# Kernel optimization log

Measured on AMD Instinct MI355X. Metric: run time of the kernel, lower is better.

## Reference

```python
import jax, jax.numpy as jnp
import numpy as np

OLD_W, OLD_H = 224, 224   # raster image spatial size (originalShape[2:])
NEW_W, NEW_H = 28, 28     # feature-grid spatial size (newShape[2:])
B, N_SV, HID = 64, 63, 512  # batch, surrounding agents (N-1), LSTM encoder hidden
POS_SCALE = 250.0         # some positions exceed OLD_W to exercise validity masks


def setup_inputs() -> dict:
    key = jax.random.key(0)
    k1, k2, k3 = jax.random.split(key, 3)
    svPositionsAtT0 = jax.random.uniform(k1, (B, N_SV, 3), dtype=jnp.float32) * POS_SCALE
    svEncoding = jax.random.normal(k2, (B, N_SV, HID), dtype=jnp.float32)
    lengths = jax.random.randint(k3, (B,), 0, N_SV, dtype=jnp.int32)
    return {"svPositionsAtT0": svPositionsAtT0, "svEncoding": svEncoding, "lengths": lengths}


def reference(svPositionsAtT0, svEncoding, lengths):
    # Faithful vectorized form of rawToRasterScaleSocialState:
    # sequential per-agent max-writes into a zero-initialized grid == scatter-max.
    b_, n_, hid = svEncoding.shape
    x = svPositionsAtT0[..., 0]                     # (B, N)
    y = svPositionsAtT0[..., 1]
    xIdx = (x * NEW_W / OLD_W).astype(jnp.int32)    # trunc toward zero, as .long()
    yIdx = (y * NEW_H / OLD_H).astype(jnp.int32)
    agent_ids = jnp.arange(n_, dtype=lengths.dtype)[None, :]
    mask = (lengths[:, None] > agent_ids) & (xIdx < NEW_W) & (yIdx < NEW_H)  # (B, N)
    # Invalid agents: write 0 (no-op since grid init is 0 and writes are max-with-0)
    enc = jnp.where(mask[..., None], svEncoding, 0.0)          # (B, N, HID)
    xI = jnp.clip(xIdx, 0, NEW_W - 1)
    yI = jnp.clip(yIdx, 0, NEW_H - 1)
    bI = jnp.broadcast_to(jnp.arange(b_)[:, None], (b_, n_))
    grid = jnp.zeros((b_, hid, NEW_W, NEW_H), dtype=svEncoding.dtype)
    grid = grid.at[bI.ravel(), :, xI.ravel(), yI.ravel()].max(enc.reshape(b_ * n_, hid))
    return grid
```

## Files before the change

kernel.cpp:

```cpp
#include <hip/hip_runtime.h>
#include <hip/hip_bf16.h>

#define NSV    63
#define HID    512
#define GW     28
#define GH     28
#define CELLS  (GW * GH)
#define HCHUNK 16
#define NTHREADS 256
#define NF4    (HCHUNK * CELLS / 4)
#define F4ROW  (CELLS / 4)

__global__ __launch_bounds__(NTHREADS)
void scatter_grid_kernel(const float* __restrict__ pos,
                         const float* __restrict__ enc,
                         const int*   __restrict__ lengths,
                         float*       __restrict__ out) {
    const int b      = blockIdx.y;
    const int h_base = blockIdx.x * HCHUNK;
    const int t      = threadIdx.x;

    __shared__ unsigned long long mask_s[CELLS];
    __shared__ float enc_s[NSV * HCHUNK];

    for (int c = t; c < CELLS; c += NTHREADS) mask_s[c] = 0ull;

    {
        const int n = t >> 2;
        const int q = t & 3;
        if (n < NSV) {
            const float4 v = ((const float4*)(enc + ((size_t)b * NSV + n) * HID + h_base))[q];
            ((float4*)(enc_s + n * HCHUNK))[q] = v;
        }
    }
    __syncthreads();

    if (t < NSV) {
        const float x = pos[((size_t)b * NSV + t) * 3 + 0];
        const float y = pos[((size_t)b * NSV + t) * 3 + 1];
        const int len = lengths[b];
        const int xi = (int)(x * 28.0f / 224.0f);
        const int yi = (int)(y * 28.0f / 224.0f);
        if ((t < len) && (xi < GW) && (yi < GH)) {
            const int xc = min(max(xi, 0), GW - 1);
            const int yc = min(max(yi, 0), GH - 1);
            atomicOr(&mask_s[xc * GH + yc], 1ull << t);
        }
    }
    __syncthreads();

    float4* d4 = (float4*)(out + ((size_t)b * HID + h_base) * CELLS);
    for (int i = t; i < NF4; i += NTHREADS) {
        const int h = i / F4ROW;
        const int c = (i - h * F4ROW) * 4;
        float4 v = make_float4(0.f, 0.f, 0.f, 0.f);
        #pragma unroll
        for (int j = 0; j < 4; ++j) {
            unsigned long long m = mask_s[c + j];
            float val = 0.f;
            while (m) {
                const int n = __ffsll(m) - 1;
                m &= m - 1;
                val = fmaxf(val, enc_s[n * HCHUNK + h]);
            }
            (&v.x)[j] = val;
        }
        d4[i] = v;
    }
}

extern "C" void kernel_launch(void* const* d_in, const int* in_sizes, int n_in,
                              void* d_out, int out_size, void* d_ws, size_t ws_size,
                              hipStream_t stream) {
    const float* pos     = (const float*)d_in[0];
    const float* enc     = (const float*)d_in[1];
    const int*   lengths = (const int*)d_in[2];
    float*       out     = (float*)d_out;

    const int B = in_sizes[2];

    dim3 grid(HID / HCHUNK, B);
    dim3 block(NTHREADS);
    scatter_grid_kernel<<<grid, block, 0, stream>>>(pos, enc, lengths, out);
}
```

Before: 118.7 us.

## Zero-fill output tiles and scatter only occupied cells via per-cell owner masks

The per-cell shared bitmask over all 784 cells is replaced by a compacted list of occupied cells. One owner thread per cell builds that cell's agent mask. Each block streams zeros over its output tile with coalesced float4 stores, then after a barrier overwrites only the occupied cells with the max-reduced encodings. This removes the per-element mask lookups and the clearing of the large shared mask. In exchange it adds uncoalesced scattered 4-byte writes to lines that were already written, and it relies on the barrier to order the zero-fill before the overwrite.

```diff
diff --git a/kernel.cpp b/kernel.cpp
--- a/kernel.cpp
+++ b/kernel.cpp
@@ -8,8 +8,9 @@
 #define CELLS  (GW * GH)
 #define HCHUNK 16
 #define NTHREADS 256
-#define NF4    (HCHUNK * CELLS / 4)
-#define F4ROW  (CELLS / 4)
+#define TILE_F4 (HCHUNK * CELLS / 4)
+#define FULL_IT (TILE_F4 / NTHREADS)
+#define REM     (TILE_F4 - FULL_IT * NTHREADS)
 
 __global__ __launch_bounds__(NTHREADS)
 void scatter_grid_kernel(const float* __restrict__ pos,
@@ -20,10 +21,13 @@
     const int h_base = blockIdx.x * HCHUNK;
     const int t      = threadIdx.x;
 
-    __shared__ unsigned long long mask_s[CELLS];
-    __shared__ float enc_s[NSV * HCHUNK];
+    __shared__ int                cell_s[NSV];
+    __shared__ float              enc_s[NSV * HCHUNK];
+    __shared__ int                cnt_s;
+    __shared__ int                tcell_s[NSV];
+    __shared__ unsigned long long tmask_s[NSV];
 
-    for (int c = t; c < CELLS; c += NTHREADS) mask_s[c] = 0ull;
+    if (t == 0) cnt_s = 0;
 
     {
         const int n = t >> 2;
@@ -33,7 +37,6 @@
             ((float4*)(enc_s + n * HCHUNK))[q] = v;
         }
     }
-    __syncthreads();
 
     if (t < NSV) {
         const float x = pos[((size_t)b * NSV + t) * 3 + 0];
@@ -41,31 +44,50 @@
         const int len = lengths[b];
         const int xi = (int)(x * 28.0f / 224.0f);
         const int yi = (int)(y * 28.0f / 224.0f);
+        int c = -1;
         if ((t < len) && (xi < GW) && (yi < GH)) {
-            const int xc = min(max(xi, 0), GW - 1);
-            const int yc = min(max(yi, 0), GH - 1);
-            atomicOr(&mask_s[xc * GH + yc], 1ull << t);
+            c = min(max(xi, 0), GW - 1) * GH + min(max(yi, 0), GH - 1);
         }
+        cell_s[t] = c;
     }
     __syncthreads();
 
+    if (t < NSV) {
+        const int c = cell_s[t];
+        if (c >= 0) {
+            bool owner = true;
+            for (int n = 0; n < t; ++n) owner &= (cell_s[n] != c);
+            if (owner) {
+                unsigned long long m = 0;
+                for (int n = t; n < NSV; ++n)
+                    if (cell_s[n] == c) m |= (1ull << n);
+                const int i = atomicAdd(&cnt_s, 1);
+                tcell_s[i] = c;
+                tmask_s[i] = m;
+            }
+        }
+    }
+
     float4* d4 = (float4*)(out + ((size_t)b * HID + h_base) * CELLS);
-    for (int i = t; i < NF4; i += NTHREADS) {
-        const int h = i / F4ROW;
-        const int c = (i - h * F4ROW) * 4;
-        float4 v = make_float4(0.f, 0.f, 0.f, 0.f);
-        #pragma unroll
-        for (int j = 0; j < 4; ++j) {
-            unsigned long long m = mask_s[c + j];
-            float val = 0.f;
-            while (m) {
-                const int n = __ffsll(m) - 1;
-                m &= m - 1;
-                val = fmaxf(val, enc_s[n * HCHUNK + h]);
-            }
-            (&v.x)[j] = val;
+    const float4 z = make_float4(0.f, 0.f, 0.f, 0.f);
+    #pragma unroll
+    for (int i = 0; i < FULL_IT; ++i) d4[t + i * NTHREADS] = z;
+    if (t < REM) d4[t + FULL_IT * NTHREADS] = z;
+
+    __syncthreads();
+
+    const int total = cnt_s * HCHUNK;
+    for (int p = t; p < total; p += NTHREADS) {
+        const int i = p >> 4;
+        const int h = p & 15;
+        unsigned long long m = tmask_s[i];
+        float val = 0.f;
+        while (m) {
+            const int n = __ffsll(m) - 1;
+            m &= m - 1;
+            val = fmaxf(val, enc_s[n * HCHUNK + h]);
         }
-        d4[i] = v;
+        out[((size_t)b * HID + h_base + h) * CELLS + tcell_s[i]] = val;
     }
 }
 
```

New measurement: 119.8 us. About the same (+1.0%).
